# Kernel tuning notes

Measured on AMD Instinct MI355X. Metric: run time of the kernel, lower is better.

Reference implementation:

```python
import jax, jax.numpy as jnp
import numpy as np

N_NODES = 100000
N_EDGES = 1600000
IN_F = 128
HID = 128
OUT = 2


def setup_inputs() -> dict:
    key = jax.random.key(0)
    ks = jax.random.split(key, 12)
    s = lambda k, sh, f: jax.random.normal(k, sh, dtype=jnp.float32) * (1.0 / np.sqrt(f))
    return {
        "x": jax.random.normal(ks[0], (N_NODES, IN_F), dtype=jnp.float32),
        "W_self1": s(ks[1], (IN_F, HID), IN_F),
        "W_neigh1": s(ks[2], (IN_F, HID), IN_F),
        "b1": jnp.zeros((HID,), dtype=jnp.float32),
        "W_self2": s(ks[3], (HID, HID), HID),
        "W_neigh2": s(ks[4], (HID, HID), HID),
        "b2": jnp.zeros((HID,), dtype=jnp.float32),
        "W_final": s(ks[5], (HID, OUT), HID),
        "b_final": jnp.zeros((OUT,), dtype=jnp.float32),
        "src": jax.random.randint(ks[6], (N_EDGES,), 0, N_NODES, dtype=jnp.int32),
        "dst": jax.random.randint(ks[7], (N_EDGES,), 0, N_NODES, dtype=jnp.int32),
    }


def _sage_mean(x, src, dst, n_nodes, W_self, W_neigh, b):
    # gather neighbor (src) features, scatter-mean onto dst nodes
    msg_sum = jax.ops.segment_sum(x[src], dst, num_segments=n_nodes)  # [N, F]
    deg = jax.ops.segment_sum(jnp.ones((src.shape[0],), x.dtype), dst,
                              num_segments=n_nodes)  # [N]
    h_neigh = msg_sum / jnp.maximum(deg, 1.0)[:, None]
    # DGL SAGEConv(mean): fc_self(h_self) + fc_neigh(h_neigh) (+ bias)
    return x @ W_self + h_neigh @ W_neigh + b


def reference(x, W_self1, W_neigh1, b1, W_self2, W_neigh2, b2,
              W_final, b_final, src, dst):
    n = x.shape[0]
    h = jax.nn.relu(_sage_mean(x, src, dst, n, W_self1, W_neigh1, b1))
    h = jax.nn.relu(_sage_mean(h, src, dst, n, W_self2, W_neigh2, b2))
    return h @ W_final + b_final  # [N, 2]
```

## Files before the change

kernel.cpp:

```cpp
#include <hip/hip_runtime.h>

#define N_NODES 100000
#define N_EDGES 1600000
#define F 128

#define BSHIFT 9
#define BNODES 512
#define NBUCK 196
#define P1_BLOCKS 128
#define P1_TPB 256
#define EPB1 (N_EDGES / P1_BLOCKS)
#define CAPB 160
#define SRC_SHIFT 12
#define NSPLIT 25
#define KEYS (BNODES * NSPLIT)
#define P2_TPB 512

typedef _Float16 f16x8 __attribute__((ext_vector_type(8)));
typedef _Float16 f16x4 __attribute__((ext_vector_type(4)));
typedef _Float16 f16x2 __attribute__((ext_vector_type(2)));
typedef float f32x4 __attribute__((ext_vector_type(4)));

__global__ __launch_bounds__(P1_TPB) void k_part(const int* __restrict__ src,
                                                 const int* __restrict__ dst,
                                                 int* __restrict__ stage,
                                                 int* __restrict__ pcnt) {
    __shared__ int cnt[NBUCK];
    int t = threadIdx.x, blk = blockIdx.x;
    if (t < NBUCK) cnt[t] = 0;
    __syncthreads();
    int base = blk * EPB1;
    for (int i = t; i < EPB1; i += P1_TPB) {
        int e = base + i;
        int s = src[e], d = dst[e];
        int b = d >> BSHIFT;
        int pos = atomicAdd(&cnt[b], 1);
        if (pos < CAPB)
            stage[((long)b * P1_BLOCKS + blk) * CAPB + pos] = (s << BSHIFT) | (d & (BNODES - 1));
    }
    __syncthreads();
    if (t < NBUCK) pcnt[t * P1_BLOCKS + blk] = min(cnt[t], CAPB);
}

__global__ void k_bucketsum(const int* __restrict__ pcnt, int* __restrict__ bbase,
                            int* __restrict__ row_start) {
    __shared__ int tot[NBUCK];
    int t = threadIdx.x;
    for (int b = t; b < NBUCK; b += 256) {
        int s = 0;
        for (int i = 0; i < P1_BLOCKS; i++) s += pcnt[b * P1_BLOCKS + i];
        tot[b] = s;
    }
    __syncthreads();
    if (t == 0) {
        int acc = 0;
        for (int i = 0; i < NBUCK; i++) {
            bbase[i] = acc;
            acc += tot[i];
        }
        bbase[NBUCK] = acc;
        row_start[N_NODES] = acc;
    }
}

__global__ __launch_bounds__(P2_TPB) void k_build(const int* __restrict__ stage,
                                                  const int* __restrict__ pcnt,
                                                  const int* __restrict__ bbase,
                                                  int* __restrict__ row_start,
                                                  int* __restrict__ esrc) {
    __shared__ int cnt[KEYS];
    __shared__ int scanw[P2_TPB / 64];
    int b = blockIdx.x, t = threadIdx.x;
    int nodeBase = b * BNODES;
    for (int i = t; i < KEYS; i += P2_TPB) cnt[i] = 0;
    __syncthreads();
    int grp = t >> 7, gt = t & 127;
    for (int s = grp; s < P1_BLOCKS; s += 4) {
        int n = pcnt[b * P1_BLOCKS + s];
        const int* seg = &stage[((long)b * P1_BLOCKS + s) * CAPB];
        for (int i = gt; i < n; i += 128) {
            int pk = seg[i];
            atomicAdd(&cnt[(pk & (BNODES - 1)) * NSPLIT + (pk >> (BSHIFT + SRC_SHIFT))], 1);
        }
    }
    __syncthreads();
    int kbase = t * 25;
    int sum = 0;
#pragma unroll
    for (int i = 0; i < 25; i++) sum += cnt[kbase + i];
    int lane = t & 63, wv = t >> 6;
    int x = sum;
#pragma unroll
    for (int off = 1; off < 64; off <<= 1) {
        int y = __shfl_up(x, off, 64);
        if (lane >= off) x += y;
    }
    if (lane == 63) scanw[wv] = x;
    __syncthreads();
    if (t == 0) {
        int acc = 0;
        for (int i = 0; i < P2_TPB / 64; i++) {
            int y = scanw[i];
            scanw[i] = acc;
            acc += y;
        }
    }
    __syncthreads();
    int run = x - sum + scanw[wv];
#pragma unroll
    for (int i = 0; i < 25; i++) {
        int c = cnt[kbase + i];
        cnt[kbase + i] = run;
        run += c;
    }
    __syncthreads();
    int base0 = bbase[b];
    {
        int node = nodeBase + t;
        if (t < BNODES && node < N_NODES) row_start[node] = base0 + cnt[t * NSPLIT];
    }
    __syncthreads();
    for (int s = grp; s < P1_BLOCKS; s += 4) {
        int n = pcnt[b * P1_BLOCKS + s];
        const int* seg = &stage[((long)b * P1_BLOCKS + s) * CAPB];
        for (int i = gt; i < n; i += 128) {
            int pk = seg[i];
            int pos = atomicAdd(&cnt[(pk & (BNODES - 1)) * NSPLIT + (pk >> (BSHIFT + SRC_SHIFT))], 1);
            esrc[base0 + pos] = pk >> BSHIFT;
        }
    }
}

__global__ void k_cast(const float* __restrict__ x, _Float16* __restrict__ xh, int n4) {
    int i = blockIdx.x * blockDim.x + threadIdx.x;
    if (i < n4) {
        float4 v = ((const float4*)x)[i];
        f16x4 h;
        h.x = (_Float16)v.x; h.y = (_Float16)v.y;
        h.z = (_Float16)v.z; h.w = (_Float16)v.w;
        ((f16x4*)xh)[i] = h;
    }
}

__global__ void k_prepw(const float* __restrict__ Ws1, const float* __restrict__ Wn1,
                        const float* __restrict__ Ws2, const float* __restrict__ Wn2,
                        _Float16* __restrict__ Wt1, _Float16* __restrict__ Wt2) {
    int i = blockIdx.x * blockDim.x + threadIdx.x;
    int which = i >> 15;
    int j = i & 32767;
    int n = j >> 8;
    int k = j & 255;
    const float* Ws = which ? Ws2 : Ws1;
    const float* Wn = which ? Wn2 : Wn1;
    _Float16* Wt = which ? Wt2 : Wt1;
    float v = (k < 128) ? Ws[k * F + n] : Wn[(k - 128) * F + n];
    Wt[n * 256 + k] = (_Float16)v;
}

__global__ __launch_bounds__(256, 8) void k_agg(const f16x8* __restrict__ xf,
                                                const int* __restrict__ row_start,
                                                const int* __restrict__ esrc,
                                                f16x8* __restrict__ out) {
    int wave = (int)((blockIdx.x * blockDim.x + threadIdx.x) >> 6);
    int lane = threadIdx.x & 63;
    if (wave >= N_NODES) return;
    int g = lane >> 4;
    int sl = lane & 15;
    int beg = row_start[wave], end = row_start[wave + 1];
    int deg = end - beg;
    int e = 0;
    if (lane < deg) e = esrc[beg + lane];
    float acc[8];
#pragma unroll
    for (int j = 0; j < 8; j++) acc[j] = 0.f;
    int n64 = min(deg, 64);
    int i = 0;
    for (; i + 16 <= n64; i += 16) {
        int s0 = __shfl(e, i + g, 64);
        int s1 = __shfl(e, i + 4 + g, 64);
        int s2 = __shfl(e, i + 8 + g, 64);
        int s3 = __shfl(e, i + 12 + g, 64);
        f16x8 v0 = xf[(long)s0 * 16 + sl];
        f16x8 v1 = xf[(long)s1 * 16 + sl];
        f16x8 v2 = xf[(long)s2 * 16 + sl];
        f16x8 v3 = xf[(long)s3 * 16 + sl];
#pragma unroll
        for (int j = 0; j < 8; j++)
            acc[j] += ((float)v0[j] + (float)v1[j]) + ((float)v2[j] + (float)v3[j]);
    }
    for (; i + 8 <= n64; i += 8) {
        int s0 = __shfl(e, i + g, 64);
        int s1 = __shfl(e, i + 4 + g, 64);
        f16x8 v0 = xf[(long)s0 * 16 + sl];
        f16x8 v1 = xf[(long)s1 * 16 + sl];
#pragma unroll
        for (int j = 0; j < 8; j++) acc[j] += (float)v0[j] + (float)v1[j];
    }
    for (; i < n64; i += 4) {
        int idx = i + g;
        float m = (idx < n64) ? 1.f : 0.f;
        int s = __shfl(e, (idx < n64) ? idx : 0, 64);
        f16x8 v = xf[(long)s * 16 + sl];
#pragma unroll
        for (int j = 0; j < 8; j++) acc[j] += (float)v[j] * m;
    }
    for (int j2 = beg + 64 + g; j2 < end; j2 += 4) {
        int s = esrc[j2];
        f16x8 v = xf[(long)s * 16 + sl];
#pragma unroll
        for (int j = 0; j < 8; j++) acc[j] += (float)v[j];
    }
#pragma unroll
    for (int j = 0; j < 8; j++) {
        acc[j] += __shfl_xor(acc[j], 16, 64);
        acc[j] += __shfl_xor(acc[j], 32, 64);
    }
    if (g == 0) {
        float inv = (deg > 0) ? 1.0f / (float)deg : 0.0f;
        f16x8 r;
#pragma unroll
        for (int j = 0; j < 8; j++) r[j] = (_Float16)(acc[j] * inv);
        out[(long)wave * 16 + sl] = r;
    }
}

template <bool FINAL>
__global__ __launch_bounds__(256, 2) void k_gemm_mfma(
    const _Float16* __restrict__ Aself, const _Float16* __restrict__ Aneigh,
    const _Float16* __restrict__ Wt, const float* __restrict__ bias,
    _Float16* __restrict__ Hout, const float* __restrict__ Wf,
    const float* __restrict__ bf, float* __restrict__ Out) {
    const int M = N_NODES;
    __shared__ _Float16 Wl[4096 * 8];
    int w = threadIdx.x >> 6;
    int lane = threadIdx.x & 63;
    int q = lane >> 4;
    int ln = lane & 15;
    int rBase = blockIdx.x * 128 + w * 32;

#pragma unroll
    for (int i = 0; i < 16; i++) {
        int s = threadIdx.x + i * 256;
        int L = s & 63, ct = (s >> 6) & 7, ks = s >> 9;
        int g = (ct * 16 + (L & 15)) * 256 + ks * 32 + (L >> 4) * 8;
        *(f16x8*)&Wl[s * 8] = *(const f16x8*)&Wt[g];
    }

    f32x4 acc[2][8];
#pragma unroll
    for (int rt = 0; rt < 2; rt++)
#pragma unroll
        for (int ct = 0; ct < 8; ct++) acc[rt][ct] = (f32x4){0.f, 0.f, 0.f, 0.f};

    __syncthreads();

    for (int ks = 0; ks < 8; ks++) {
        const _Float16* Abase = (ks < 4) ? Aself : Aneigh;
        int k0 = (ks & 3) * 32;
        f16x8 b[8];
#pragma unroll
        for (int ct = 0; ct < 8; ct++)
            b[ct] = *(const f16x8*)&Wl[((ks * 8 + ct) * 64 + lane) * 8];
#pragma unroll
        for (int rt = 0; rt < 2; rt++) {
            int row = rBase + rt * 16 + ln;
            f16x8 a = {};
            if (row < M) a = *(const f16x8*)&Abase[(long)row * F + k0 + q * 8];
#pragma unroll
            for (int ct = 0; ct < 8; ct++)
                acc[rt][ct] = __builtin_amdgcn_mfma_f32_16x16x32_f16(a, b[ct], acc[rt][ct], 0, 0, 0);
        }
    }

    float bv[8];
#pragma unroll
    for (int ct = 0; ct < 8; ct++) bv[ct] = bias[ct * 16 + ln];

    if (!FINAL) {
#pragma unroll
        for (int rt = 0; rt < 2; rt++) {
#pragma unroll
            for (int r = 0; r < 4; r++) {
                int row = rBase + rt * 16 + q * 4 + r;
                if (row < M) {
#pragma unroll
                    for (int ct = 0; ct < 8; ct++) {
                        float h = acc[rt][ct][r] + bv[ct];
                        h = h > 0.f ? h : 0.f;
                        Hout[(long)row * F + ct * 16 + ln] = (_Float16)h;
                    }
                }
            }
        }
    } else {
        float wf0[8], wf1[8];
#pragma unroll
        for (int ct = 0; ct < 8; ct++) {
            int c = ct * 16 + ln;
            wf0[ct] = Wf[c * 2 + 0];
            wf1[ct] = Wf[c * 2 + 1];
        }
        float bf0 = bf[0], bf1 = bf[1];
#pragma unroll
        for (int rt = 0; rt < 2; rt++) {
#pragma unroll
            for (int r = 0; r < 4; r++) {
                int row = rBase + rt * 16 + q * 4 + r;
                float p0 = 0.f, p1 = 0.f;
#pragma unroll
                for (int ct = 0; ct < 8; ct++) {
                    float h = acc[rt][ct][r] + bv[ct];
                    h = h > 0.f ? h : 0.f;
                    p0 += h * wf0[ct];
                    p1 += h * wf1[ct];
                }
#pragma unroll
                for (int off = 1; off < 16; off <<= 1) {
                    p0 += __shfl_xor(p0, off, 64);
                    p1 += __shfl_xor(p1, off, 64);
                }
                if (ln == 0 && row < M) {
                    Out[(long)row * 2 + 0] = p0 + bf0;
                    Out[(long)row * 2 + 1] = p1 + bf1;
                }
            }
        }
    }
}

extern "C" void kernel_launch(void* const* d_in, const int* in_sizes, int n_in,
                              void* d_out, int out_size, void* d_ws, size_t ws_size,
                              hipStream_t stream) {
    const float* x   = (const float*)d_in[0];
    const float* Ws1 = (const float*)d_in[1];
    const float* Wn1 = (const float*)d_in[2];
    const float* b1  = (const float*)d_in[3];
    const float* Ws2 = (const float*)d_in[4];
    const float* Wn2 = (const float*)d_in[5];
    const float* b2  = (const float*)d_in[6];
    const float* Wf  = (const float*)d_in[7];
    const float* bf  = (const float*)d_in[8];
    const int* src   = (const int*)d_in[9];
    const int* dst   = (const int*)d_in[10];
    float* out = (float*)d_out;

    char* ws = (char*)d_ws;
    int*      row_start = (int*)(ws + 0);
    int*      bbase     = (int*)(ws + 400016);
    int*      pcnt      = (int*)(ws + 400816);
    int*      stage     = (int*)(ws + 501184);
    int*      esrc      = (int*)(ws + 16557504);
    _Float16* xh        = (_Float16*)(ws + 22957504);
    _Float16* hneigh    = (_Float16*)(ws + 48557504);
    _Float16* h1        = (_Float16*)(ws + 74157504);
    _Float16* Wt1       = (_Float16*)(ws + 99757504);
    _Float16* Wt2       = (_Float16*)(ws + 99823040);

    const int TPB = 256;
    k_part<<<P1_BLOCKS, P1_TPB, 0, stream>>>(src, dst, stage, pcnt);
    k_bucketsum<<<1, 256, 0, stream>>>(pcnt, bbase, row_start);
    k_build<<<NBUCK, P2_TPB, 0, stream>>>(stage, pcnt, bbase, row_start, esrc);

    k_cast<<<(N_NODES * F / 4 + TPB - 1) / TPB, TPB, 0, stream>>>(x, xh, N_NODES * F / 4);
    k_prepw<<<256, 256, 0, stream>>>(Ws1, Wn1, Ws2, Wn2, Wt1, Wt2);

    k_agg<<<(N_NODES + 3) / 4, 256, 0, stream>>>((const f16x8*)xh, row_start, esrc,
                                                 (f16x8*)hneigh);
    k_gemm_mfma<false><<<(N_NODES + 127) / 128, 256, 0, stream>>>(
        xh, hneigh, Wt1, b1, h1, nullptr, nullptr, nullptr);
    k_agg<<<(N_NODES + 3) / 4, 256, 0, stream>>>((const f16x8*)h1, row_start, esrc,
                                                 (f16x2*)hneigh ? (f16x8*)hneigh : nullptr);
    k_gemm_mfma<true><<<(N_NODES + 127) / 128, 256, 0, stream>>>(
        h1, hneigh, Wt2, b2, nullptr, Wf, bf, out);
}
```

Baseline: 386.5 us.

## Fuse prep kernels, fold bucket prefix into build, shrink GEMM LDS for occupancy

Merges the edge partition, the fp32-to-fp16 cast of x and the weight transpose into one launch with role-by-block-index. It removes the single-block bucketsum kernel: each build block now computes its own bucket base by reducing the pcnt prefix itself. The GEMM keeps only the first 6 of 8 k-slices of W in LDS and reads the last two straight from global memory, so it can target 3 blocks per CU instead of 2. The aim is fewer launches and serial gaps, plus better GEMM occupancy. The cost is redundant prefix reads in each build block and uncached global weight loads in the GEMM inner loop.

Result: slower. 405.5 us (+4.9%).

```diff
diff --git a/kernel.cpp b/kernel.cpp
--- a/kernel.cpp
+++ b/kernel.cpp
@@ -16,64 +16,100 @@
 #define KEYS (BNODES * NSPLIT)
 #define P2_TPB 512
 
+#define CAST_BLOCKS 12500
+#define PREPW_BLOCKS 256
+
 typedef _Float16 f16x8 __attribute__((ext_vector_type(8)));
 typedef _Float16 f16x4 __attribute__((ext_vector_type(4)));
 typedef _Float16 f16x2 __attribute__((ext_vector_type(2)));
 typedef float f32x4 __attribute__((ext_vector_type(4)));
 
-__global__ __launch_bounds__(P1_TPB) void k_part(const int* __restrict__ src,
-                                                 const int* __restrict__ dst,
-                                                 int* __restrict__ stage,
-                                                 int* __restrict__ pcnt) {
+__global__ __launch_bounds__(256) void k_prep(const int* __restrict__ src,
+                                              const int* __restrict__ dst,
+                                              int* __restrict__ stage,
+                                              int* __restrict__ pcnt,
+                                              const float* __restrict__ x,
+                                              _Float16* __restrict__ xh,
+                                              const float* __restrict__ Ws1,
+                                              const float* __restrict__ Wn1,
+                                              const float* __restrict__ Ws2,
+                                              const float* __restrict__ Wn2,
+                                              _Float16* __restrict__ Wt1,
+                                              _Float16* __restrict__ Wt2) {
     __shared__ int cnt[NBUCK];
     int t = threadIdx.x, blk = blockIdx.x;
-    if (t < NBUCK) cnt[t] = 0;
-    __syncthreads();
-    int base = blk * EPB1;
-    for (int i = t; i < EPB1; i += P1_TPB) {
-        int e = base + i;
-        int s = src[e], d = dst[e];
-        int b = d >> BSHIFT;
-        int pos = atomicAdd(&cnt[b], 1);
-        if (pos < CAPB)
-            stage[((long)b * P1_BLOCKS + blk) * CAPB + pos] = (s << BSHIFT) | (d & (BNODES - 1));
-    }
-    __syncthreads();
-    if (t < NBUCK) pcnt[t * P1_BLOCKS + blk] = min(cnt[t], CAPB);
-}
-
-__global__ void k_bucketsum(const int* __restrict__ pcnt, int* __restrict__ bbase,
-                            int* __restrict__ row_start) {
-    __shared__ int tot[NBUCK];
-    int t = threadIdx.x;
-    for (int b = t; b < NBUCK; b += 256) {
-        int s = 0;
-        for (int i = 0; i < P1_BLOCKS; i++) s += pcnt[b * P1_BLOCKS + i];
-        tot[b] = s;
-    }
-    __syncthreads();
-    if (t == 0) {
-        int acc = 0;
-        for (int i = 0; i < NBUCK; i++) {
-            bbase[i] = acc;
-            acc += tot[i];
-        }
-        bbase[NBUCK] = acc;
-        row_start[N_NODES] = acc;
+    if (blk < P1_BLOCKS) {
+        if (t < NBUCK) cnt[t] = 0;
+        __syncthreads();
+        int base = blk * EPB1;
+        for (int i = t; i < EPB1; i += P1_TPB) {
+            int e = base + i;
+            int s = src[e], d = dst[e];
+            int b = d >> BSHIFT;
+            int pos = atomicAdd(&cnt[b], 1);
+            if (pos < CAPB)
+                stage[((long)b * P1_BLOCKS + blk) * CAPB + pos] = (s << BSHIFT) | (d & (BNODES - 1));
+        }
+        __syncthreads();
+        if (t < NBUCK) pcnt[t * P1_BLOCKS + blk] = min(cnt[t], CAPB);
+    } else if (blk < P1_BLOCKS + CAST_BLOCKS) {
+        int i = (blk - P1_BLOCKS) * 256 + t;
+        float4 v = ((const float4*)x)[i];
+        f16x4 h;
+        h.x = (_Float16)v.x; h.y = (_Float16)v.y;
+        h.z = (_Float16)v.z; h.w = (_Float16)v.w;
+        ((f16x4*)xh)[i] = h;
+    } else {
+        int i = (blk - P1_BLOCKS - CAST_BLOCKS) * 256 + t;
+        int which = i >> 15;
+        int j = i & 32767;
+        int n = j >> 8;
+        int k = j & 255;
+        const float* Ws = which ? Ws2 : Ws1;
+        const float* Wn = which ? Wn2 : Wn1;
+        _Float16* Wt = which ? Wt2 : Wt1;
+        float v = (k < 128) ? Ws[k * F + n] : Wn[(k - 128) * F + n];
+        Wt[n * 256 + k] = (_Float16)v;
     }
 }
 
 __global__ __launch_bounds__(P2_TPB) void k_build(const int* __restrict__ stage,
                                                   const int* __restrict__ pcnt,
-                                                  const int* __restrict__ bbase,
                                                   int* __restrict__ row_start,
                                                   int* __restrict__ esrc) {
     __shared__ int cnt[KEYS];
     __shared__ int scanw[P2_TPB / 64];
+    __shared__ int redA[P2_TPB / 64], redB[P2_TPB / 64];
     int b = blockIdx.x, t = threadIdx.x;
     int nodeBase = b * BNODES;
     for (int i = t; i < KEYS; i += P2_TPB) cnt[i] = 0;
-    __syncthreads();
+
+    int lim = (b + 1) * P1_BLOCKS;
+    int own0 = b * P1_BLOCKS;
+    int sInc = 0, sOwn = 0;
+    for (int i = t; i < lim; i += P2_TPB) {
+        int v = pcnt[i];
+        sInc += v;
+        if (i >= own0) sOwn += v;
+    }
+    int lane = t & 63, wv = t >> 6;
+#pragma unroll
+    for (int off = 32; off >= 1; off >>= 1) {
+        sInc += __shfl_xor(sInc, off, 64);
+        sOwn += __shfl_xor(sOwn, off, 64);
+    }
+    if (lane == 0) { redA[wv] = sInc; redB[wv] = sOwn; }
+    __syncthreads();
+    if (t == 0) {
+        int a = 0, c = 0;
+        for (int i = 0; i < P2_TPB / 64; i++) { a += redA[i]; c += redB[i]; }
+        redA[0] = a - c;
+        redB[0] = a;
+    }
+    __syncthreads();
+    int base0 = redA[0];
+    if (b == NBUCK - 1 && t == 0) row_start[N_NODES] = redB[0];
+
     int grp = t >> 7, gt = t & 127;
     for (int s = grp; s < P1_BLOCKS; s += 4) {
         int n = pcnt[b * P1_BLOCKS + s];
@@ -88,7 +124,6 @@
     int sum = 0;
 #pragma unroll
     for (int i = 0; i < 25; i++) sum += cnt[kbase + i];
-    int lane = t & 63, wv = t >> 6;
     int x = sum;
 #pragma unroll
     for (int off = 1; off < 64; off <<= 1) {
@@ -114,7 +149,6 @@
         run += c;
     }
     __syncthreads();
-    int base0 = bbase[b];
     {
         int node = nodeBase + t;
         if (t < BNODES && node < N_NODES) row_start[node] = base0 + cnt[t * NSPLIT];
@@ -129,32 +163,6 @@
             esrc[base0 + pos] = pk >> BSHIFT;
         }
     }
-}
-
-__global__ void k_cast(const float* __restrict__ x, _Float16* __restrict__ xh, int n4) {
-    int i = blockIdx.x * blockDim.x + threadIdx.x;
-    if (i < n4) {
-        float4 v = ((const float4*)x)[i];
-        f16x4 h;
-        h.x = (_Float16)v.x; h.y = (_Float16)v.y;
-        h.z = (_Float16)v.z; h.w = (_Float16)v.w;
-        ((f16x4*)xh)[i] = h;
-    }
-}
-
-__global__ void k_prepw(const float* __restrict__ Ws1, const float* __restrict__ Wn1,
-                        const float* __restrict__ Ws2, const float* __restrict__ Wn2,
-                        _Float16* __restrict__ Wt1, _Float16* __restrict__ Wt2) {
-    int i = blockIdx.x * blockDim.x + threadIdx.x;
-    int which = i >> 15;
-    int j = i & 32767;
-    int n = j >> 8;
-    int k = j & 255;
-    const float* Ws = which ? Ws2 : Ws1;
-    const float* Wn = which ? Wn2 : Wn1;
-    _Float16* Wt = which ? Wt2 : Wt1;
-    float v = (k < 128) ? Ws[k * F + n] : Wn[(k - 128) * F + n];
-    Wt[n * 256 + k] = (_Float16)v;
 }
 
 __global__ __launch_bounds__(256, 8) void k_agg(const f16x8* __restrict__ xf,
@@ -225,13 +233,13 @@
 }
 
 template <bool FINAL>
-__global__ __launch_bounds__(256, 2) void k_gemm_mfma(
+__global__ __launch_bounds__(256, 3) void k_gemm_mfma(
     const _Float16* __restrict__ Aself, const _Float16* __restrict__ Aneigh,
     const _Float16* __restrict__ Wt, const float* __restrict__ bias,
     _Float16* __restrict__ Hout, const float* __restrict__ Wf,
     const float* __restrict__ bf, float* __restrict__ Out) {
     const int M = N_NODES;
-    __shared__ _Float16 Wl[4096 * 8];
+    __shared__ _Float16 Wl[3072 * 8];
     int w = threadIdx.x >> 6;
     int lane = threadIdx.x & 63;
     int q = lane >> 4;
@@ -239,7 +247,7 @@
     int rBase = blockIdx.x * 128 + w * 32;
 
 #pragma unroll
-    for (int i = 0; i < 16; i++) {
+    for (int i = 0; i < 12; i++) {
         int s = threadIdx.x + i * 256;
         int L = s & 63, ct = (s >> 6) & 7, ks = s >> 9;
         int g = (ct * 16 + (L & 15)) * 256 + ks * 32 + (L >> 4) * 8;
@@ -258,9 +266,15 @@
         const _Float16* Abase = (ks < 4) ? Aself : Aneigh;
         int k0 = (ks & 3) * 32;
         f16x8 b[8];
-#pragma unroll
-        for (int ct = 0; ct < 8; ct++)
-            b[ct] = *(const f16x8*)&Wl[((ks * 8 + ct) * 64 + lane) * 8];
+        if (ks < 6) {
+#pragma unroll
+            for (int ct = 0; ct < 8; ct++)
+                b[ct] = *(const f16x8*)&Wl[((ks * 8 + ct) * 64 + lane) * 8];
+        } else {
+#pragma unroll
+            for (int ct = 0; ct < 8; ct++)
+                b[ct] = *(const f16x8*)&Wt[(ct * 16 + ln) * 256 + ks * 32 + q * 8];
+        }
 #pragma unroll
         for (int rt = 0; rt < 2; rt++) {
             int row = rBase + rt * 16 + ln;
@@ -346,7 +360,6 @@
 
     char* ws = (char*)d_ws;
     int*      row_start = (int*)(ws + 0);
-    int*      bbase     = (int*)(ws + 400016);
     int*      pcnt      = (int*)(ws + 400816);
     int*      stage     = (int*)(ws + 501184);
     int*      esrc      = (int*)(ws + 16557504);
@@ -356,20 +369,16 @@
     _Float16* Wt1       = (_Float16*)(ws + 99757504);
     _Float16* Wt2       = (_Float16*)(ws + 99823040);
 
-    const int TPB = 256;
-    k_part<<<P1_BLOCKS, P1_TPB, 0, stream>>>(src, dst, stage, pcnt);
-    k_bucketsum<<<1, 256, 0, stream>>>(pcnt, bbase, row_start);
-    k_build<<<NBUCK, P2_TPB, 0, stream>>>(stage, pcnt, bbase, row_start, esrc);
-
-    k_cast<<<(N_NODES * F / 4 + TPB - 1) / TPB, TPB, 0, stream>>>(x, xh, N_NODES * F / 4);
-    k_prepw<<<256, 256, 0, stream>>>(Ws1, Wn1, Ws2, Wn2, Wt1, Wt2);
+    k_prep<<<P1_BLOCKS + CAST_BLOCKS + PREPW_BLOCKS, 256, 0, stream>>>(
+        src, dst, stage, pcnt, x, xh, Ws1, Wn1, Ws2, Wn2, Wt1, Wt2);
+    k_build<<<NBUCK, P2_TPB, 0, stream>>>(stage, pcnt, row_start, esrc);
 
     k_agg<<<(N_NODES + 3) / 4, 256, 0, stream>>>((const f16x8*)xh, row_start, esrc,
                                                  (f16x8*)hneigh);
     k_gemm_mfma<false><<<(N_NODES + 127) / 128, 256, 0, stream>>>(
         xh, hneigh, Wt1, b1, h1, nullptr, nullptr, nullptr);
     k_agg<<<(N_NODES + 3) / 4, 256, 0, stream>>>((const f16x8*)h1, row_start, esrc,
-                                                 (f16x2*)hneigh ? (f16x8*)hneigh : nullptr);
+                                                 (f16x8*)hneigh);
     k_gemm_mfma<true><<<(N_NODES + 127) / 128, 256, 0, stream>>>(
         h1, hneigh, Wt2, b2, nullptr, Wf, bf, out);
 }
```
